# Optimization experiments

Hardware: AMD Instinct MI355X
Metric: run time of the kernel (lower is better)

Reference implementation:

```python
import math
import jax, jax.numpy as jnp
import numpy as np

QDEPTH = 8
WIDTH = 32
HEIGHT = 32
PIXELS = WIDTH * HEIGHT          # 1024
WIRES = int(math.ceil(math.log2(PIXELS)))  # 10, and PIXELS == 2**WIRES exactly
BATCH = 2048


def setup_inputs() -> dict:
    key = jax.random.key(0)
    k1, k2 = jax.random.split(key)
    x = jax.random.normal(k1, (BATCH, 1, WIDTH, HEIGHT), dtype=jnp.float32)
    # torch.randn(weight_shape) * 0.4
    weights = jax.random.normal(k2, (QDEPTH, WIRES, 3), dtype=jnp.float32) * 0.4
    return {"x": x, "weights": weights, "reps": 1}


def _apply_1q(s, U, wire):
    # s: (batch, 2, 2, ..., 2); apply 2x2 unitary U on qubit `wire` (axis wire+1)
    ax = wire + 1
    s = jnp.moveaxis(s, ax, -1)
    s = s @ U.T                      # new[..., i] = sum_j U[i, j] * old[..., j]
    return jnp.moveaxis(s, -1, ax)


def _apply_cnot(s, ctrl, tgt):
    # flip target bit on the control==1 half of the state
    c_ax = ctrl + 1
    t_ax = tgt + 1
    s0 = jnp.take(s, 0, axis=c_ax)
    s1 = jnp.take(s, 1, axis=c_ax)
    t = t_ax - 1 if t_ax > c_ax else t_ax
    s1 = jnp.flip(s1, axis=t)
    return jnp.stack([s0, s1], axis=c_ax)


def _rot_matrix(phi, theta, omega):
    # qml.Rot = RZ(phi) -> RY(theta) -> RZ(omega)
    c = jnp.cos(theta * 0.5)
    sn = jnp.sin(theta * 0.5)
    ep = jnp.exp(-0.5j * (phi + omega))   # e^{-i(phi+omega)/2}
    em = jnp.exp(-0.5j * (phi - omega))   # e^{-i(phi-omega)/2}
    return jnp.stack([
        jnp.stack([ep * c, -jnp.conj(em) * sn]),
        jnp.stack([em * sn, jnp.conj(ep) * c]),
    ]).astype(jnp.complex64)


def _circuit(psi, weights, reps):
    # psi: (batch, 2**WIRES) complex64 normalized state
    b = psi.shape[0]
    s = psi.reshape((b,) + (2,) * WIRES)
    w = jnp.tanh(weights)                 # qw_map.tanh
    # StronglyEntanglingLayers default ranges: r_l = l % (wires-1) + 1
    ranges = [(l % (WIRES - 1)) + 1 for l in range(QDEPTH)]
    for _ in range(reps):
        for l in range(QDEPTH):
            for q in range(WIRES):
                U = _rot_matrix(w[l, q, 0], w[l, q, 1], w[l, q, 2])
                s = _apply_1q(s, U, q)
            r = ranges[l]
            for q in range(WIRES):
                s = _apply_cnot(s, q, (q + r) % WIRES)
    return s.reshape(b, 2 ** WIRES)


def reference(x, weights, reps):
    b = x.shape[0]
    v = x.reshape(b, PIXELS)                       # b 1 w h -> b (w h)
    old_norm = jnp.linalg.norm(v, axis=-1, keepdims=True)
    psi = (v / old_norm).astype(jnp.complex64)     # real amplitudes, zero imag
    out = _circuit(psi, weights, reps)
    out = out * old_norm.astype(jnp.complex64)
    return out.reshape(b, 1, WIDTH, HEIGHT)
```

## Files before the change

### kernel.cpp

```cpp
#include <hip/hip_runtime.h>
#include <math.h>


#define WIRES   10
#define NSTATE  1024
#define QDEPTH  8
#define NBATCH  2048
#define NGATES  (QDEPTH * WIRES)

typedef float v2f __attribute__((ext_vector_type(2)));

#define WS_WORDS 1280

__device__ __forceinline__ int perm_g(int j, int r) {
#pragma unroll
    for (int q = WIRES - 1; q >= 0; --q) {
        const int cb = 9 - q;
        const int tb = 9 - ((q + r) % WIRES);
        j ^= ((j >> cb) & 1) << tb;
    }
    return j;
}

__global__ __launch_bounds__(1024) void qprep(
    const float* __restrict__ weights, float* __restrict__ ws)
{
    const int tid = threadIdx.x;
    if (tid < NGATES) {
        const float phi   = tanhf(weights[tid * 3 + 0]);
        const float theta = tanhf(weights[tid * 3 + 1]);
        const float omega = tanhf(weights[tid * 3 + 2]);
        const float c  = cosf(theta * 0.5f);
        const float sn = sinf(theta * 0.5f);
        const float a  = 0.5f * (phi + omega);
        const float bb = 0.5f * (phi - omega);
        const float ca = cosf(a),  sa = sinf(a);
        const float cb = cosf(bb), sb = sinf(bb);
        ws[tid * 8 + 0] =  ca * c;  ws[tid * 8 + 1] = -sa * c;
        ws[tid * 8 + 2] = -cb * sn; ws[tid * 8 + 3] = -sb * sn;
        ws[tid * 8 + 4] =  cb * sn; ws[tid * 8 + 5] = -sb * sn;
        ws[tid * 8 + 6] =  ca * c;  ws[tid * 8 + 7] =  sa * c;
    }
    int* wsI = (int*)ws;
    if (tid >= 128 && tid < 256) {
        const int e = tid - 128, l = e >> 4, t = e & 15;
        const int j = perm_g(t, (l % (WIRES - 1)) + 1);
        wsI[640 + e] = ((j & 15) << 6) | (j >> 4);
    }
    if (tid >= 256 && tid < 768) {
        const int e = tid - 256, l = e >> 6, v = e & 63;
        const int j = perm_g(v << 4, (l % (WIRES - 1)) + 1);
        wsI[768 + e] = ((j & 15) << 6) | (j >> 4);
    }
}

template<int CTRL>
__device__ __forceinline__ float dppmov(float x) {
    return __int_as_float(__builtin_amdgcn_update_dpp(
        0, __float_as_int(x), CTRL, 0xF, 0xF, true));
}
#define FX1(v)  dppmov<0xB1>(v)
#define FX2(v)  dppmov<0x4E>(v)
#define FX4(v)  dppmov<0x1B>(dppmov<0x141>(v))
#define FX8(v)  dppmov<0x128>(v)
#define FX16(v) __shfl_xor((v), 16, 64)
#define FX32(v) __shfl_xor((v), 32, 64)

#define APPLY_LOCAL(uptr, mask)                                               \
    {                                                                         \
        const float* __restrict__ u = (uptr);                                 \
        const float u00r=u[0], u00i=u[1], u01r=u[2], u01i=u[3];               \
        const float u10r=u[4], u10i=u[5], u11r=u[6], u11i=u[7];               \
        _Pragma("unroll")                                                     \
        for (int t0 = 0; t0 < 16; ++t0) {                                     \
            if (t0 & (mask)) continue;                                        \
            const int t1 = t0 | (mask);                                       \
            const v2f a0 = z[t0], a1 = z[t1];                                 \
            const v2f j0 = (v2f){-a0.y, a0.x};                                \
            const v2f j1 = (v2f){-a1.y, a1.x};                                \
            z[t0] = a0*u00r + j0*u00i + a1*u01r + j1*u01i;                    \
            z[t1] = a0*u10r + j0*u10i + a1*u11r + j1*u11i;                    \
        }                                                                     \
    }

#define LANE_GATE(W, J, FETCH)                                                \
    {                                                                         \
        const float* __restrict__ u = gw + (W) * 8;                           \
        const bool hi = (lane >> (J)) & 1;                                    \
        const float c0r = hi ? u[6] : u[0], c0i = hi ? u[7] : u[1];           \
        const float c1r = hi ? u[4] : u[2], c1i = hi ? u[5] : u[3];           \
        _Pragma("unroll")                                                     \
        for (int t = 0; t < 16; ++t) {                                        \
            v2f p;                                                            \
            p.x = FETCH(z[t].x);                                              \
            p.y = FETCH(z[t].y);                                              \
            const v2f s  = z[t];                                              \
            const v2f js = (v2f){-s.y, s.x};                                  \
            const v2f jp = (v2f){-p.y, p.x};                                  \
            z[t] = s*c0r + js*c0i + p*c1r + jp*c1i;                           \
        }                                                                     \
    }

__global__ __launch_bounds__(64) void qsim_wave(
    const float* __restrict__ x,
    const float* __restrict__ ws,
    float* __restrict__ out,
    const int interleaved)
{
    __shared__ float lre[NSTATE];
    __shared__ float lim[NSTATE];
    const int lane = threadIdx.x;
    const int b    = blockIdx.x;
    const int* __restrict__ wsI = (const int*)ws;

    v2f z[16];

    const float4* __restrict__ x4 =
        (const float4*)(x + ((size_t)b << 10) + (lane << 4));
#pragma unroll
    for (int k = 0; k < 4; ++k) {
        const float4 v = x4[k];
        z[4*k+0] = (v2f){v.x, 0.f};
        z[4*k+1] = (v2f){v.y, 0.f};
        z[4*k+2] = (v2f){v.z, 0.f};
        z[4*k+3] = (v2f){v.w, 0.f};
    }

    for (int l = 0; l < QDEPTH; ++l) {
        const float* __restrict__ gw = ws + l * 80;

        APPLY_LOCAL(gw + 9*8, 1)
        APPLY_LOCAL(gw + 8*8, 2)
        APPLY_LOCAL(gw + 7*8, 4)
        APPLY_LOCAL(gw + 6*8, 8)

        LANE_GATE(5, 0, FX1)
        LANE_GATE(4, 1, FX2)
        LANE_GATE(3, 2, FX4)
        LANE_GATE(2, 3, FX8)
        LANE_GATE(1, 4, FX16)
        LANE_GATE(0, 5, FX32)

#pragma unroll
        for (int t = 0; t < 16; ++t) {
            lre[t * 64 + lane] = z[t].x;
            lim[t * 64 + lane] = z[t].y;
        }
        const int ga = wsI[768 + l * 64 + lane];
#pragma unroll
        for (int t = 0; t < 16; ++t) {
            const int a = ga ^ wsI[640 + l * 16 + t];
            z[t] = (v2f){lre[a], lim[a]};
        }
    }

    if (interleaved) {
        float2* __restrict__ o2 = (float2*)out;
#pragma unroll
        for (int t = 0; t < 16; ++t)
            o2[((size_t)b << 10) + (lane << 4) + t] = make_float2(z[t].x, z[t].y);
    } else {
        float4* __restrict__ o4 = (float4*)(out + ((size_t)b << 10) + (lane << 4));
#pragma unroll
        for (int k = 0; k < 4; ++k)
            o4[k] = make_float4(z[4*k+0].x, z[4*k+1].x, z[4*k+2].x, z[4*k+3].x);
    }
}

__global__ __launch_bounds__(256) void qcircuit_kernel(
    const float* __restrict__ x, const float* __restrict__ weights,
    float* __restrict__ out, const int interleaved)
{
    __shared__ float s_re[NSTATE];
    __shared__ float s_im[NSTATE];
    __shared__ float s_g[NGATES][8];
    const int tid = threadIdx.x;
    const int b   = blockIdx.x;
    if (tid < NGATES) {
        const float phi   = tanhf(weights[tid * 3 + 0]);
        const float theta = tanhf(weights[tid * 3 + 1]);
        const float omega = tanhf(weights[tid * 3 + 2]);
        const float c  = cosf(theta * 0.5f);
        const float sn = sinf(theta * 0.5f);
        const float a  = 0.5f * (phi + omega);
        const float bb = 0.5f * (phi - omega);
        const float ca = cosf(a),  sa = sinf(a);
        const float cb = cosf(bb), sb = sinf(bb);
        s_g[tid][0] =  ca * c;  s_g[tid][1] = -sa * c;
        s_g[tid][2] = -cb * sn; s_g[tid][3] = -sb * sn;
        s_g[tid][4] =  cb * sn; s_g[tid][5] = -sb * sn;
        s_g[tid][6] =  ca * c;  s_g[tid][7] =  sa * c;
    }
#pragma unroll
    for (int k = 0; k < 4; ++k) {
        const int i = tid + 256 * k;
        s_re[i] = x[b * NSTATE + i];
        s_im[i] = 0.0f;
    }
    __syncthreads();
    for (int l = 0; l < QDEPTH; ++l) {
        for (int q = 0; q < WIRES; ++q) {
            const int gi = l * WIRES + q;
            const float u00r = s_g[gi][0], u00i = s_g[gi][1];
            const float u01r = s_g[gi][2], u01i = s_g[gi][3];
            const float u10r = s_g[gi][4], u10i = s_g[gi][5];
            const float u11r = s_g[gi][6], u11i = s_g[gi][7];
            const int sh = 9 - q;
            const int m  = 1 << sh;
#pragma unroll
            for (int k = 0; k < 2; ++k) {
                const int p  = tid + 256 * k;
                const int i0 = ((p >> sh) << (sh + 1)) | (p & (m - 1));
                const int i1 = i0 | m;
                const float a0r = s_re[i0], a0i = s_im[i0];
                const float a1r = s_re[i1], a1i = s_im[i1];
                s_re[i0] = u00r*a0r - u00i*a0i + u01r*a1r - u01i*a1i;
                s_im[i0] = u00r*a0i + u00i*a0r + u01r*a1i + u01i*a1r;
                s_re[i1] = u10r*a0r - u10i*a0i + u11r*a1r - u11i*a1i;
                s_im[i1] = u10r*a0i + u10i*a0r + u11r*a1i + u11i*a1r;
            }
            __syncthreads();
        }
        const int r = (l % (WIRES - 1)) + 1;
        float vr[4], vi[4];
#pragma unroll
        for (int k = 0; k < 4; ++k) {
            const int i = tid + 256 * k;
            const int j = perm_g(i, r);
            vr[k] = s_re[j]; vi[k] = s_im[j];
        }
        __syncthreads();
#pragma unroll
        for (int k = 0; k < 4; ++k) {
            const int i = tid + 256 * k;
            s_re[i] = vr[k]; s_im[i] = vi[k];
        }
        __syncthreads();
    }
    if (interleaved) {
#pragma unroll
        for (int k = 0; k < 4; ++k) {
            const int i  = tid + 256 * k;
            const int fi = 2 * (b * NSTATE + i);
            out[fi + 0] = s_re[i];
            out[fi + 1] = s_im[i];
        }
    } else {
#pragma unroll
        for (int k = 0; k < 4; ++k) {
            const int i = tid + 256 * k;
            out[b * NSTATE + i] = s_re[i];
        }
    }
}

extern "C" void kernel_launch(void* const* d_in, const int* in_sizes, int n_in,
                              void* d_out, int out_size, void* d_ws, size_t ws_size,
                              hipStream_t stream) {
    const float* x       = (const float*)d_in[0];
    const float* weights = (const float*)d_in[1];
    float* out = (float*)d_out;
    const int interleaved = (out_size >= 2 * NBATCH * NSTATE) ? 1 : 0;

    if (ws_size >= WS_WORDS * sizeof(float)) {
        float* ws = (float*)d_ws;
        qprep<<<1, 1024, 0, stream>>>(weights, ws);
        qsim_wave<<<NBATCH, 64, 0, stream>>>(x, ws, out, interleaved);
    } else {
        qcircuit_kernel<<<NBATCH, 256, 0, stream>>>(x, weights, out, interleaved);
    }
}
```

Baseline: 117.0 us.

## Repack wave state into split real/imag pairs for packed FP32 math

```diff
diff --git a/kernel.cpp b/kernel.cpp
--- a/kernel.cpp
+++ b/kernel.cpp
@@ -9,6 +9,7 @@
 #define NGATES  (QDEPTH * WIRES)
 
 typedef float v2f __attribute__((ext_vector_type(2)));
+static __device__ __forceinline__ v2f s2(float x) { return (v2f){x, x}; }
 
 #define WS_WORDS 1280
 
@@ -66,38 +67,38 @@
 #define FX16(v) __shfl_xor((v), 16, 64)
 #define FX32(v) __shfl_xor((v), 32, 64)
 
-#define APPLY_LOCAL(uptr, mask)                                               \
+#define APPLY_LOCAL_PK(uptr, mask)                                            \
     {                                                                         \
         const float* __restrict__ u = (uptr);                                 \
         const float u00r=u[0], u00i=u[1], u01r=u[2], u01i=u[3];               \
         const float u10r=u[4], u10i=u[5], u11r=u[6], u11i=u[7];               \
         _Pragma("unroll")                                                     \
-        for (int t0 = 0; t0 < 16; ++t0) {                                     \
-            if (t0 & (mask)) continue;                                        \
-            const int t1 = t0 | (mask);                                       \
-            const v2f a0 = z[t0], a1 = z[t1];                                 \
-            const v2f j0 = (v2f){-a0.y, a0.x};                                \
-            const v2f j1 = (v2f){-a1.y, a1.x};                                \
-            z[t0] = a0*u00r + j0*u00i + a1*u01r + j1*u01i;                    \
-            z[t1] = a0*u10r + j0*u10i + a1*u11r + j1*u11i;                    \
+        for (int k0 = 0; k0 < 8; ++k0) {                                      \
+            if (k0 & (mask)) continue;                                        \
+            const int k1 = k0 | (mask);                                       \
+            const v2f a0r = zr[k0], a0i = zi[k0];                             \
+            const v2f a1r = zr[k1], a1i = zi[k1];                             \
+            zr[k0] = s2(u00r)*a0r - s2(u00i)*a0i + s2(u01r)*a1r - s2(u01i)*a1i;\
+            zi[k0] = s2(u00r)*a0i + s2(u00i)*a0r + s2(u01r)*a1i + s2(u01i)*a1r;\
+            zr[k1] = s2(u10r)*a0r - s2(u10i)*a0i + s2(u11r)*a1r - s2(u11i)*a1i;\
+            zi[k1] = s2(u10r)*a0i + s2(u10i)*a0r + s2(u11r)*a1i + s2(u11i)*a1r;\
         }                                                                     \
     }
 
-#define LANE_GATE(W, J, FETCH)                                                \
+#define LANE_GATE_PK(W, J, FETCH)                                             \
     {                                                                         \
         const float* __restrict__ u = gw + (W) * 8;                           \
         const bool hi = (lane >> (J)) & 1;                                    \
         const float c0r = hi ? u[6] : u[0], c0i = hi ? u[7] : u[1];           \
         const float c1r = hi ? u[4] : u[2], c1i = hi ? u[5] : u[3];           \
         _Pragma("unroll")                                                     \
-        for (int t = 0; t < 16; ++t) {                                        \
-            v2f p;                                                            \
-            p.x = FETCH(z[t].x);                                              \
-            p.y = FETCH(z[t].y);                                              \
-            const v2f s  = z[t];                                              \
-            const v2f js = (v2f){-s.y, s.x};                                  \
-            const v2f jp = (v2f){-p.y, p.x};                                  \
-            z[t] = s*c0r + js*c0i + p*c1r + jp*c1i;                           \
+        for (int k = 0; k < 8; ++k) {                                         \
+            v2f pr, pi;                                                       \
+            pr.x = FETCH(zr[k].x); pr.y = FETCH(zr[k].y);                     \
+            pi.x = FETCH(zi[k].x); pi.y = FETCH(zi[k].y);                     \
+            const v2f sr = zr[k], si = zi[k];                                 \
+            zr[k] = s2(c0r)*sr - s2(c0i)*si + s2(c1r)*pr - s2(c1i)*pi;        \
+            zi[k] = s2(c0r)*si + s2(c0i)*sr + s2(c1r)*pi + s2(c1i)*pr;        \
         }                                                                     \
     }
 
@@ -113,57 +114,81 @@
     const int b    = blockIdx.x;
     const int* __restrict__ wsI = (const int*)ws;
 
-    v2f z[16];
+    v2f zr[8], zi[8];
 
     const float4* __restrict__ x4 =
         (const float4*)(x + ((size_t)b << 10) + (lane << 4));
-#pragma unroll
-    for (int k = 0; k < 4; ++k) {
-        const float4 v = x4[k];
-        z[4*k+0] = (v2f){v.x, 0.f};
-        z[4*k+1] = (v2f){v.y, 0.f};
-        z[4*k+2] = (v2f){v.z, 0.f};
-        z[4*k+3] = (v2f){v.w, 0.f};
+    {
+        const float4 v0 = x4[0], v1 = x4[1], v2 = x4[2], v3 = x4[3];
+        zr[0].x=v0.x; zr[1].x=v0.y; zr[2].x=v0.z; zr[3].x=v0.w;
+        zr[4].x=v1.x; zr[5].x=v1.y; zr[6].x=v1.z; zr[7].x=v1.w;
+        zr[0].y=v2.x; zr[1].y=v2.y; zr[2].y=v2.z; zr[3].y=v2.w;
+        zr[4].y=v3.x; zr[5].y=v3.y; zr[6].y=v3.z; zr[7].y=v3.w;
+#pragma unroll
+        for (int k = 0; k < 8; ++k) zi[k] = (v2f){0.f, 0.f};
     }
 
     for (int l = 0; l < QDEPTH; ++l) {
         const float* __restrict__ gw = ws + l * 80;
 
-        APPLY_LOCAL(gw + 9*8, 1)
-        APPLY_LOCAL(gw + 8*8, 2)
-        APPLY_LOCAL(gw + 7*8, 4)
-        APPLY_LOCAL(gw + 6*8, 8)
-
-        LANE_GATE(5, 0, FX1)
-        LANE_GATE(4, 1, FX2)
-        LANE_GATE(3, 2, FX4)
-        LANE_GATE(2, 3, FX8)
-        LANE_GATE(1, 4, FX16)
-        LANE_GATE(0, 5, FX32)
-
-#pragma unroll
-        for (int t = 0; t < 16; ++t) {
-            lre[t * 64 + lane] = z[t].x;
-            lim[t * 64 + lane] = z[t].y;
+        APPLY_LOCAL_PK(gw + 9*8, 1)
+        APPLY_LOCAL_PK(gw + 8*8, 2)
+        APPLY_LOCAL_PK(gw + 7*8, 4)
+
+        {
+            const float* __restrict__ u = gw + 6*8;
+            const v2f pAr = (v2f){u[0], u[6]};
+            const v2f pAi = (v2f){u[1], u[7]};
+            const v2f pBr = (v2f){u[2], u[4]};
+            const v2f pBi = (v2f){u[3], u[5]};
+#pragma unroll
+            for (int k = 0; k < 8; ++k) {
+                const v2f r  = zr[k], i = zi[k];
+                const v2f rs = __builtin_shufflevector(r, r, 1, 0);
+                const v2f is = __builtin_shufflevector(i, i, 1, 0);
+                zr[k] = pAr*r - pAi*i + pBr*rs - pBi*is;
+                zi[k] = pAr*i + pAi*r + pBr*is + pBi*rs;
+            }
+        }
+
+        LANE_GATE_PK(5, 0, FX1)
+        LANE_GATE_PK(4, 1, FX2)
+        LANE_GATE_PK(3, 2, FX4)
+        LANE_GATE_PK(2, 3, FX8)
+        LANE_GATE_PK(1, 4, FX16)
+        LANE_GATE_PK(0, 5, FX32)
+
+#pragma unroll
+        for (int k = 0; k < 8; ++k) {
+            lre[k * 64 + lane]         = zr[k].x;
+            lre[(k + 8) * 64 + lane]   = zr[k].y;
+            lim[k * 64 + lane]         = zi[k].x;
+            lim[(k + 8) * 64 + lane]   = zi[k].y;
         }
         const int ga = wsI[768 + l * 64 + lane];
 #pragma unroll
-        for (int t = 0; t < 16; ++t) {
-            const int a = ga ^ wsI[640 + l * 16 + t];
-            z[t] = (v2f){lre[a], lim[a]};
+        for (int k = 0; k < 8; ++k) {
+            const int a0 = ga ^ wsI[640 + l * 16 + k];
+            const int a1 = ga ^ wsI[640 + l * 16 + k + 8];
+            zr[k].x = lre[a0]; zi[k].x = lim[a0];
+            zr[k].y = lre[a1]; zi[k].y = lim[a1];
         }
     }
 
     if (interleaved) {
         float2* __restrict__ o2 = (float2*)out;
-#pragma unroll
-        for (int t = 0; t < 16; ++t)
-            o2[((size_t)b << 10) + (lane << 4) + t] = make_float2(z[t].x, z[t].y);
+        const size_t base = ((size_t)b << 10) + (lane << 4);
+#pragma unroll
+        for (int k = 0; k < 8; ++k) {
+            o2[base + k]     = make_float2(zr[k].x, zi[k].x);
+            o2[base + k + 8] = make_float2(zr[k].y, zi[k].y);
+        }
     } else {
         float4* __restrict__ o4 = (float4*)(out + ((size_t)b << 10) + (lane << 4));
-#pragma unroll
-        for (int k = 0; k < 4; ++k)
-            o4[k] = make_float4(z[4*k+0].x, z[4*k+1].x, z[4*k+2].x, z[4*k+3].x);
+        o4[0] = make_float4(zr[0].x, zr[1].x, zr[2].x, zr[3].x);
+        o4[1] = make_float4(zr[4].x, zr[5].x, zr[6].x, zr[7].x);
+        o4[2] = make_float4(zr[0].y, zr[1].y, zr[2].y, zr[3].y);
+        o4[3] = make_float4(zr[4].y, zr[5].y, zr[6].y, zr[7].y);
     }
 }
 
```

Result: faster. 104.1 us, median of 3 (-11.0%).
